# Performance work log

Measured on AMD Instinct MI355X. Metric: run time of the kernel, lower is better.

## Reference

```python
import jax, jax.numpy as jnp
import numpy as np

H = 1024          # h_dim
FF = 4 * H
E = 8             # num_expert
TOP_K = 2


def setup_inputs() -> dict:
    key = jax.random.key(0)
    ks = jax.random.split(key, 7)
    B, S = 4, 2048
    s = 0.02
    return {
        "x": jax.random.normal(ks[0], (B, S, H), dtype=jnp.float32),
        "Wg": jax.random.normal(ks[1], (H, E), dtype=jnp.float32) * s,
        "bg": jnp.zeros((E,), dtype=jnp.float32),
        "W1": jax.random.normal(ks[2], (E, H, FF), dtype=jnp.float32) * s,
        "b1": jnp.zeros((E, FF), dtype=jnp.float32),
        "W2": jax.random.normal(ks[3], (E, FF, H), dtype=jnp.float32) * s,
        "b2": jnp.zeros((E, H), dtype=jnp.float32),
    }


def _moe(x, Wg, bg, W1, b1, W2, b2):
    B, S, h = x.shape
    hs = x.reshape(-1, h)                                  # [T, H]
    logits = hs @ Wg + bg                                  # [T, E]
    probs = jax.nn.softmax(logits.astype(jnp.float32), axis=-1)
    w, idx = jax.lax.top_k(probs, TOP_K)                   # [T, K]
    w = jax.nn.softmax(w, axis=-1).astype(x.dtype)         # renormalize over top-k
    out = jnp.zeros_like(hs)
    for e in range(E):
        # per-token combine weight for expert e (0 if not selected)
        w_e = jnp.sum(w * (idx == e), axis=-1)             # [T]
        y = jax.nn.relu(hs @ W1[e] + b1[e]) @ W2[e] + b2[e]  # [T, H]
        out = out + w_e[:, None] * y
    return out.reshape(B, S, h), logits


def reference(x, Wg, bg, W1, b1, W2, b2):
    return _moe(x, Wg, bg, W1, b1, W2, b2)
```

## Files before the change

kernel.cpp:

```cpp
#include <hip/hip_runtime.h>
#include <hip/hip_bf16.h>

#define T_TOKENS 8192
#define HD 1024
#define FF 4096
#define NEXP 8
#define NR_MAX 17408

typedef __attribute__((ext_vector_type(8))) short bf16x8;
typedef __attribute__((ext_vector_type(4))) float f32x4;
typedef unsigned short ushort8v __attribute__((ext_vector_type(8)));

static __device__ __forceinline__ float b2f(ushort u) {
    union { unsigned u; float f; } c; c.u = ((unsigned)u) << 16; return c.f;
}
static __device__ __forceinline__ ushort f2b(float f) {
    union { float f; unsigned u; } c; c.f = f;
    unsigned r = c.u + 0x7fffu + ((c.u >> 16) & 1u);
    return (ushort)(r >> 16);
}

__global__ __launch_bounds__(256) void gate_kernel(
    const float* __restrict__ x, const float* __restrict__ Wg, const float* __restrict__ bg,
    float* __restrict__ logits, int* __restrict__ counts,
    int* __restrict__ e0a, int* __restrict__ e1a,
    float* __restrict__ w0a, float* __restrict__ w1a)
{
    int t = blockIdx.x * 4 + (threadIdx.x >> 6);
    int l = threadIdx.x & 63;
    const float* xr = x + (size_t)t * HD;
    float acc[8] = {0,0,0,0,0,0,0,0};
    #pragma unroll
    for (int i = 0; i < 4; ++i) {
        int h0 = i * 256 + l * 4;
        float4 xv = *(const float4*)(xr + h0);
        #pragma unroll
        for (int j = 0; j < 4; ++j) {
            float xs = (&xv.x)[j];
            const float4* wr = (const float4*)(Wg + (size_t)(h0 + j) * NEXP);
            float4 wa = wr[0], wb = wr[1];
            acc[0] = fmaf(xs, wa.x, acc[0]);
            acc[1] = fmaf(xs, wa.y, acc[1]);
            acc[2] = fmaf(xs, wa.z, acc[2]);
            acc[3] = fmaf(xs, wa.w, acc[3]);
            acc[4] = fmaf(xs, wb.x, acc[4]);
            acc[5] = fmaf(xs, wb.y, acc[5]);
            acc[6] = fmaf(xs, wb.z, acc[6]);
            acc[7] = fmaf(xs, wb.w, acc[7]);
        }
    }
    #pragma unroll
    for (int off = 32; off > 0; off >>= 1) {
        #pragma unroll
        for (int e = 0; e < 8; ++e) acc[e] += __shfl_down(acc[e], off, 64);
    }
    if (l == 0) {
        float lg[8];
        #pragma unroll
        for (int e = 0; e < 8; ++e) {
            lg[e] = acc[e] + bg[e];
            logits[(size_t)t * NEXP + e] = lg[e];
        }
        float m = lg[0];
        #pragma unroll
        for (int e = 1; e < 8; ++e) m = fmaxf(m, lg[e]);
        float p[8], s = 0.f;
        #pragma unroll
        for (int e = 0; e < 8; ++e) { p[e] = expf(lg[e] - m); s += p[e]; }
        float inv = 1.f / s;
        #pragma unroll
        for (int e = 0; e < 8; ++e) p[e] *= inv;
        int i0 = 0;
        #pragma unroll
        for (int e = 1; e < 8; ++e) if (p[e] > p[i0]) i0 = e;
        int i1 = (i0 == 0) ? 1 : 0;
        #pragma unroll
        for (int e = 0; e < 8; ++e) if (e != i0 && p[e] > p[i1]) i1 = e;
        float ed = expf(p[i1] - p[i0]);
        float w0 = 1.f / (1.f + ed);
        float w1 = ed / (1.f + ed);
        e0a[t] = i0; e1a[t] = i1; w0a[t] = w0; w1a[t] = w1;
        atomicAdd(&counts[i0], 1);
        atomicAdd(&counts[i1], 1);
    }
}

__global__ void offsets_kernel(const int* __restrict__ counts, int* __restrict__ off) {
    if (threadIdx.x == 0) {
        int o = 0;
        for (int e = 0; e < 8; ++e) { off[e] = o; o += (counts[e] + 127) & ~127; }
        off[8] = o;
    }
}

__global__ __launch_bounds__(256) void assign_kernel(
    const int* __restrict__ e0a, const int* __restrict__ e1a,
    const int* __restrict__ off, int* __restrict__ fill,
    int* __restrict__ row0, int* __restrict__ row1, int* __restrict__ row_token)
{
    int t = blockIdx.x * 256 + threadIdx.x;
    if (t >= T_TOKENS) return;
    int e0 = e0a[t];
    int r0 = off[e0] + atomicAdd(&fill[e0], 1);
    row0[t] = r0; row_token[r0] = t;
    int e1 = e1a[t];
    int r1 = off[e1] + atomicAdd(&fill[e1], 1);
    row1[t] = r1; row_token[r1] = t;
}

__global__ __launch_bounds__(256) void gather_kernel(
    const float* __restrict__ x, const int* __restrict__ row_token, ushort* __restrict__ Xp)
{
    int r = blockIdx.x;
    int tok = row_token[r];
    int c = threadIdx.x * 4;
    ushort4 o;
    if (tok >= 0 && tok < T_TOKENS) {
        float4 v = *(const float4*)(x + (size_t)tok * HD + c);
        o.x = f2b(v.x); o.y = f2b(v.y); o.z = f2b(v.z); o.w = f2b(v.w);
    } else {
        o.x = 0; o.y = 0; o.z = 0; o.w = 0;
    }
    *(ushort4*)(Xp + (size_t)r * HD + c) = o;
}

__global__ __launch_bounds__(256) void transpose_cvt_kernel(
    const float* __restrict__ in, ushort* __restrict__ out, int R, int C)
{
    __shared__ ushort tile[64][65];
    size_t esz = (size_t)R * C;
    const float* ein = in + (size_t)blockIdx.z * esz;
    ushort* eout = out + (size_t)blockIdx.z * esz;
    int c0 = blockIdx.x * 64, r0 = blockIdx.y * 64;
    int tr = threadIdx.x >> 4;
    int tc = (threadIdx.x & 15) * 4;
    #pragma unroll
    for (int i = 0; i < 4; ++i) {
        int r = tr + i * 16;
        float4 v = *(const float4*)(ein + (size_t)(r0 + r) * C + c0 + tc);
        tile[r][tc + 0] = f2b(v.x);
        tile[r][tc + 1] = f2b(v.y);
        tile[r][tc + 2] = f2b(v.z);
        tile[r][tc + 3] = f2b(v.w);
    }
    __syncthreads();
    int twc = threadIdx.x >> 3;
    int twr = (threadIdx.x & 7) * 8;
    #pragma unroll
    for (int i = 0; i < 2; ++i) {
        int cc = twc + i * 32;
        ushort8v v;
        #pragma unroll
        for (int j = 0; j < 8; ++j) v[j] = tile[twr + j][cc];
        *(ushort8v*)(eout + (size_t)(c0 + cc) * R + r0 + twr) = v;
    }
}

template<int K, int NTOT, bool RELU>
__global__ __launch_bounds__(256) void gemm_kernel(
    const ushort* __restrict__ A, const ushort* __restrict__ Bt,
    const float* __restrict__ bias, ushort* __restrict__ Out,
    const int* __restrict__ off)
{
    constexpr int NT = NTOT / 128;
    __shared__ __align__(16) ushort lds[2][2][128 * 32];

    int nwg = gridDim.x;
    int bid = blockIdx.x;
    int wgid = (bid & 7) * (nwg >> 3) + (bid >> 3);
    int ntile = wgid % NT;
    int mtile = wgid / NT;
    int r0 = mtile * 128;
    int total = off[8];
    if (r0 >= total) return;
    int e = 0;
    #pragma unroll
    for (int q = 0; q < 7; ++q) if (r0 >= off[q + 1]) e = q + 1;

    int tid = threadIdx.x;
    int w = tid >> 6, lane = tid & 63;
    int wr = w >> 1, wc = w & 1;
    int lr = lane & 15, lk = lane >> 4;

    const ushort* Ab = A + (size_t)r0 * K;
    const ushort* Bb = Bt + ((size_t)e * NTOT + (size_t)ntile * 128) * K;

    auto stage = [&](const ushort* gbase, ushort* ldsbase) {
        #pragma unroll
        for (int issue = 0; issue < 2; ++issue) {
            int row = issue * 64 + w * 16 + (lane >> 2);
            int chunk = (lane & 3) ^ ((lane >> 3) & 3);
            const ushort* g = gbase + (size_t)row * K + chunk * 8;
            ushort* lp = ldsbase + (issue * 64 + w * 16) * 32;
            __builtin_amdgcn_global_load_lds(
                (const __attribute__((address_space(1))) void*)g,
                (__attribute__((address_space(3))) void*)lp, 16, 0, 0);
        }
    };

    stage(Ab, &lds[0][0][0]);
    stage(Bb, &lds[0][1][0]);

    f32x4 acc[4][4];
    #pragma unroll
    for (int mi = 0; mi < 4; ++mi)
        #pragma unroll
        for (int ni = 0; ni < 4; ++ni) acc[mi][ni] = (f32x4){0.f, 0.f, 0.f, 0.f};

    __syncthreads();

    constexpr int KT = K / 32;
    int cur = 0;
    int slot = lk ^ ((lr >> 1) & 3);
    for (int kt = 0; kt < KT; ++kt) {
        if (kt + 1 < KT) {
            stage(Ab + (kt + 1) * 32, &lds[cur ^ 1][0][0]);
            stage(Bb + (kt + 1) * 32, &lds[cur ^ 1][1][0]);
        }
        const ushort* As = &lds[cur][0][0];
        const ushort* Bs = &lds[cur][1][0];
        bf16x8 a[4], b[4];
        #pragma unroll
        for (int mi = 0; mi < 4; ++mi)
            a[mi] = *(const bf16x8*)(As + (wr * 64 + mi * 16 + lr) * 32 + slot * 8);
        #pragma unroll
        for (int ni = 0; ni < 4; ++ni)
            b[ni] = *(const bf16x8*)(Bs + (wc * 64 + ni * 16 + lr) * 32 + slot * 8);
        #pragma unroll
        for (int mi = 0; mi < 4; ++mi)
            #pragma unroll
            for (int ni = 0; ni < 4; ++ni)
                acc[mi][ni] = __builtin_amdgcn_mfma_f32_16x16x32_bf16(
                    a[mi], b[ni], acc[mi][ni], 0, 0, 0);
        __syncthreads();
        cur ^= 1;
    }

    int c0 = ntile * 128 + wc * 64;
    int rbase = r0 + wr * 64;
    #pragma unroll
    for (int ni = 0; ni < 4; ++ni) {
        int n = c0 + ni * 16 + lr;
        float bv = bias[(size_t)e * NTOT + n];
        #pragma unroll
        for (int mi = 0; mi < 4; ++mi) {
            int m = rbase + mi * 16 + lk * 4;
            #pragma unroll
            for (int j = 0; j < 4; ++j) {
                float v = acc[mi][ni][j] + bv;
                if (RELU) v = fmaxf(v, 0.f);
                Out[(size_t)(m + j) * NTOT + n] = f2b(v);
            }
        }
    }
}

__global__ __launch_bounds__(256) void combine_kernel(
    const ushort* __restrict__ Y, const int* __restrict__ row0, const int* __restrict__ row1,
    const float* __restrict__ w0a, const float* __restrict__ w1a, float* __restrict__ out)
{
    int t = blockIdx.x;
    int c = threadIdx.x * 4;
    int r0 = row0[t], r1 = row1[t];
    float w0 = w0a[t], w1 = w1a[t];
    ushort4 ya = *(const ushort4*)(Y + (size_t)r0 * HD + c);
    ushort4 yb = *(const ushort4*)(Y + (size_t)r1 * HD + c);
    float4 o;
    o.x = w0 * b2f(ya.x) + w1 * b2f(yb.x);
    o.y = w0 * b2f(ya.y) + w1 * b2f(yb.y);
    o.z = w0 * b2f(ya.z) + w1 * b2f(yb.z);
    o.w = w0 * b2f(ya.w) + w1 * b2f(yb.w);
    *(float4*)(out + (size_t)t * HD + c) = o;
}

#define WSA(x) (((x) + 255) & ~(size_t)255)
static constexpr size_t OFF_COUNTS = 0;
static constexpr size_t OFF_FILL   = 64;
static constexpr size_t OFF_OFF    = 128;
static constexpr size_t OFF_E0     = 256;
static constexpr size_t OFF_E1     = OFF_E0 + (size_t)T_TOKENS * 4;
static constexpr size_t OFF_W0     = OFF_E1 + (size_t)T_TOKENS * 4;
static constexpr size_t OFF_W1A    = OFF_W0 + (size_t)T_TOKENS * 4;
static constexpr size_t OFF_R0     = OFF_W1A + (size_t)T_TOKENS * 4;
static constexpr size_t OFF_R1     = OFF_R0 + (size_t)T_TOKENS * 4;
static constexpr size_t OFF_RT     = OFF_R1 + (size_t)T_TOKENS * 4;
static constexpr size_t OFF_XP     = WSA(OFF_RT + (size_t)NR_MAX * 4);
static constexpr size_t OFF_W1T    = OFF_XP  + (size_t)NR_MAX * HD * 2;
static constexpr size_t OFF_W2T    = OFF_W1T + (size_t)NEXP * FF * HD * 2;
static constexpr size_t OFF_H1     = OFF_W2T + (size_t)NEXP * HD * FF * 2;
static constexpr size_t OFF_Y      = OFF_H1  + (size_t)NR_MAX * FF * 2;
static constexpr size_t WS_NEEDED  = OFF_Y   + (size_t)NR_MAX * HD * 2;

extern "C" void kernel_launch(void* const* d_in, const int* in_sizes, int n_in,
                              void* d_out, int out_size, void* d_ws, size_t ws_size,
                              hipStream_t stream) {
    (void)in_sizes; (void)n_in; (void)out_size;
    const float* x  = (const float*)d_in[0];
    const float* Wg = (const float*)d_in[1];
    const float* bg = (const float*)d_in[2];
    const float* W1 = (const float*)d_in[3];
    const float* b1 = (const float*)d_in[4];
    const float* W2 = (const float*)d_in[5];
    const float* b2 = (const float*)d_in[6];
    float* out    = (float*)d_out;
    float* logits = out + (size_t)T_TOKENS * HD;

    if (ws_size < WS_NEEDED) return;

    char* ws = (char*)d_ws;
    int*    counts = (int*)(ws + OFF_COUNTS);
    int*    fill   = (int*)(ws + OFF_FILL);
    int*    offp   = (int*)(ws + OFF_OFF);
    int*    e0a    = (int*)(ws + OFF_E0);
    int*    e1a    = (int*)(ws + OFF_E1);
    float*  w0a    = (float*)(ws + OFF_W0);
    float*  w1a    = (float*)(ws + OFF_W1A);
    int*    row0   = (int*)(ws + OFF_R0);
    int*    row1   = (int*)(ws + OFF_R1);
    int*    rowtok = (int*)(ws + OFF_RT);
    ushort* Xp     = (ushort*)(ws + OFF_XP);
    ushort* W1T    = (ushort*)(ws + OFF_W1T);
    ushort* W2T    = (ushort*)(ws + OFF_W2T);
    ushort* H1     = (ushort*)(ws + OFF_H1);
    ushort* Y      = (ushort*)(ws + OFF_Y);

    hipMemsetAsync(ws, 0, 256, stream);
    hipMemsetAsync(rowtok, 0xFF, (size_t)NR_MAX * 4, stream);

    gate_kernel<<<T_TOKENS / 4, 256, 0, stream>>>(x, Wg, bg, logits, counts, e0a, e1a, w0a, w1a);
    offsets_kernel<<<1, 64, 0, stream>>>(counts, offp);
    assign_kernel<<<T_TOKENS / 256, 256, 0, stream>>>(e0a, e1a, offp, fill, row0, row1, rowtok);
    gather_kernel<<<NR_MAX, 256, 0, stream>>>(x, rowtok, Xp);
    transpose_cvt_kernel<<<dim3(FF / 64, HD / 64, NEXP), 256, 0, stream>>>(W1, W1T, HD, FF);
    transpose_cvt_kernel<<<dim3(HD / 64, FF / 64, NEXP), 256, 0, stream>>>(W2, W2T, FF, HD);
    gemm_kernel<HD, FF, true>
        <<<(FF / 128) * (NR_MAX / 128), 256, 0, stream>>>(Xp, W1T, b1, H1, offp);
    gemm_kernel<FF, HD, false>
        <<<(HD / 128) * (NR_MAX / 128), 256, 0, stream>>>(H1, W2T, b2, Y, offp);
    combine_kernel<<<T_TOKENS, 256, 0, stream>>>(Y, row0, row1, w0a, w1a, out);
}
```

Baseline: 780.5 us.

## Widen GEMM tile to 128x256 with 512 threads and nontemporal H1 stores

The grouped expert GEMMs now use 128x256 output tiles computed by 8 waves (512 threads) instead of 128x128 with 4 waves. The B-operand staging is reworked into separate A and B LDS buffers with per-thread async global-to-LDS loads. Each loaded A tile is reused across twice as many output columns, which cuts redundant activation reads. The first GEMM also writes H1 with nontemporal stores. The trade is more LDS per block and fewer blocks per CU, and H1 may fall out of cache before the second GEMM reads it.

```diff
diff --git a/kernel.cpp b/kernel.cpp
--- a/kernel.cpp
+++ b/kernel.cpp
@@ -156,14 +156,16 @@
     }
 }
 
-template<int K, int NTOT, bool RELU>
-__global__ __launch_bounds__(256) void gemm_kernel(
+template<int K, int NTOT, bool RELU, bool NTSTORE>
+__global__ __launch_bounds__(512) void gemm_kernel(
     const ushort* __restrict__ A, const ushort* __restrict__ Bt,
     const float* __restrict__ bias, ushort* __restrict__ Out,
     const int* __restrict__ off)
 {
-    constexpr int NT = NTOT / 128;
-    __shared__ __align__(16) ushort lds[2][2][128 * 32];
+    constexpr int BN = 256;
+    constexpr int NT = NTOT / BN;
+    __shared__ __align__(16) ushort ldsA[2][128 * 32];
+    __shared__ __align__(16) ushort ldsB[2][BN * 32];
 
     int nwg = gridDim.x;
     int bid = blockIdx.x;
@@ -178,28 +180,33 @@
     for (int q = 0; q < 7; ++q) if (r0 >= off[q + 1]) e = q + 1;
 
     int tid = threadIdx.x;
-    int w = tid >> 6, lane = tid & 63;
-    int wr = w >> 1, wc = w & 1;
+    int wid = tid >> 6, lane = tid & 63;
+    int wr = wid >> 2, wc = wid & 3;
     int lr = lane & 15, lk = lane >> 4;
 
     const ushort* Ab = A + (size_t)r0 * K;
-    const ushort* Bb = Bt + ((size_t)e * NTOT + (size_t)ntile * 128) * K;
-
-    auto stage = [&](const ushort* gbase, ushort* ldsbase) {
-        #pragma unroll
-        for (int issue = 0; issue < 2; ++issue) {
-            int row = issue * 64 + w * 16 + (lane >> 2);
-            int chunk = (lane & 3) ^ ((lane >> 3) & 3);
-            const ushort* g = gbase + (size_t)row * K + chunk * 8;
-            ushort* lp = ldsbase + (issue * 64 + w * 16) * 32;
+    const ushort* Bb = Bt + ((size_t)e * NTOT + (size_t)ntile * BN) * K;
+
+    int srow = tid >> 2;
+    int schunk = (tid & 3) ^ ((tid >> 3) & 3);
+
+    auto stageA = [&](int kt, int buf) {
+        const ushort* g = Ab + (size_t)kt * 32 + (size_t)srow * K + schunk * 8;
+        __builtin_amdgcn_global_load_lds(
+            (const __attribute__((address_space(1))) void*)g,
+            (__attribute__((address_space(3))) void*)&ldsA[buf][tid * 8], 16, 0, 0);
+    };
+    auto stageB = [&](int kt, int buf) {
+        #pragma unroll
+        for (int i = 0; i < 2; ++i) {
+            const ushort* g = Bb + (size_t)kt * 32 + (size_t)(i * 128 + srow) * K + schunk * 8;
             __builtin_amdgcn_global_load_lds(
                 (const __attribute__((address_space(1))) void*)g,
-                (__attribute__((address_space(3))) void*)lp, 16, 0, 0);
+                (__attribute__((address_space(3))) void*)&ldsB[buf][i * 4096 + tid * 8], 16, 0, 0);
         }
     };
 
-    stage(Ab, &lds[0][0][0]);
-    stage(Bb, &lds[0][1][0]);
+    stageA(0, 0); stageB(0, 0);
 
     f32x4 acc[4][4];
     #pragma unroll
@@ -213,12 +220,9 @@
     int cur = 0;
     int slot = lk ^ ((lr >> 1) & 3);
     for (int kt = 0; kt < KT; ++kt) {
-        if (kt + 1 < KT) {
-            stage(Ab + (kt + 1) * 32, &lds[cur ^ 1][0][0]);
-            stage(Bb + (kt + 1) * 32, &lds[cur ^ 1][1][0]);
-        }
-        const ushort* As = &lds[cur][0][0];
-        const ushort* Bs = &lds[cur][1][0];
+        if (kt + 1 < KT) { stageA(kt + 1, cur ^ 1); stageB(kt + 1, cur ^ 1); }
+        const ushort* As = &ldsA[cur][0];
+        const ushort* Bs = &ldsB[cur][0];
         bf16x8 a[4], b[4];
         #pragma unroll
         for (int mi = 0; mi < 4; ++mi)
@@ -236,7 +240,7 @@
         cur ^= 1;
     }
 
-    int c0 = ntile * 128 + wc * 64;
+    int c0 = ntile * BN + wc * 64;
     int rbase = r0 + wr * 64;
     #pragma unroll
     for (int ni = 0; ni < 4; ++ni) {
@@ -249,7 +253,9 @@
             for (int j = 0; j < 4; ++j) {
                 float v = acc[mi][ni][j] + bv;
                 if (RELU) v = fmaxf(v, 0.f);
-                Out[(size_t)(m + j) * NTOT + n] = f2b(v);
+                ushort* p = &Out[(size_t)(m + j) * NTOT + n];
+                if (NTSTORE) __builtin_nontemporal_store(f2b(v), p);
+                else *p = f2b(v);
             }
         }
     }
@@ -333,9 +339,9 @@
     gather_kernel<<<NR_MAX, 256, 0, stream>>>(x, rowtok, Xp);
     transpose_cvt_kernel<<<dim3(FF / 64, HD / 64, NEXP), 256, 0, stream>>>(W1, W1T, HD, FF);
     transpose_cvt_kernel<<<dim3(HD / 64, FF / 64, NEXP), 256, 0, stream>>>(W2, W2T, FF, HD);
-    gemm_kernel<HD, FF, true>
-        <<<(FF / 128) * (NR_MAX / 128), 256, 0, stream>>>(Xp, W1T, b1, H1, offp);
-    gemm_kernel<FF, HD, false>
-        <<<(HD / 128) * (NR_MAX / 128), 256, 0, stream>>>(H1, W2T, b2, Y, offp);
+    gemm_kernel<HD, FF, true, true>
+        <<<(FF / 256) * (NR_MAX / 128), 512, 0, stream>>>(Xp, W1T, b1, H1, offp);
+    gemm_kernel<FF, HD, false, false>
+        <<<(HD / 256) * (NR_MAX / 128), 512, 0, stream>>>(H1, W2T, b2, Y, offp);
     combine_kernel<<<T_TOKENS, 256, 0, stream>>>(Y, row0, row1, w0a, w1a, out);
 }
```

New measurement: 893.3 us. 14.5% more time.

## Triple-buffer GEMM LDS tiles with two-deep prefetch and partial vmcnt waits

Applied to the files above, without the earlier changes.

The expert GEMM kernel moves from double-buffered to triple-buffered LDS staging. Global-to-LDS loads are now issued two K-steps ahead. Each step waits only until the next tile has landed (vmcnt(4)) instead of draining all loads with __syncthreads, so more memory latency can hide behind the MFMA work. The cost is LDS use per block rising from 32KB to 48KB, which may lower occupancy. The code also now relies on hand-written waitcnt and barrier ordering being correct.

```diff
diff --git a/kernel.cpp b/kernel.cpp
--- a/kernel.cpp
+++ b/kernel.cpp
@@ -163,7 +163,8 @@
     const int* __restrict__ off)
 {
     constexpr int NT = NTOT / 128;
-    __shared__ __align__(16) ushort lds[2][2][128 * 32];
+    constexpr int KT = K / 32;
+    __shared__ __align__(16) ushort lds[3][2][128 * 32];
 
     int nwg = gridDim.x;
     int bid = blockIdx.x;
@@ -185,38 +186,40 @@
     const ushort* Ab = A + (size_t)r0 * K;
     const ushort* Bb = Bt + ((size_t)e * NTOT + (size_t)ntile * 128) * K;
 
-    auto stage = [&](const ushort* gbase, ushort* ldsbase) {
+    auto stage = [&](int kt, int sl) {
         #pragma unroll
         for (int issue = 0; issue < 2; ++issue) {
             int row = issue * 64 + w * 16 + (lane >> 2);
             int chunk = (lane & 3) ^ ((lane >> 3) & 3);
-            const ushort* g = gbase + (size_t)row * K + chunk * 8;
-            ushort* lp = ldsbase + (issue * 64 + w * 16) * 32;
+            const ushort* ga = Ab + (size_t)kt * 32 + (size_t)row * K + chunk * 8;
+            const ushort* gb = Bb + (size_t)kt * 32 + (size_t)row * K + chunk * 8;
+            ushort* la = &lds[sl][0][(issue * 64 + w * 16) * 32];
+            ushort* lb = &lds[sl][1][(issue * 64 + w * 16) * 32];
             __builtin_amdgcn_global_load_lds(
-                (const __attribute__((address_space(1))) void*)g,
-                (__attribute__((address_space(3))) void*)lp, 16, 0, 0);
+                (const __attribute__((address_space(1))) void*)ga,
+                (__attribute__((address_space(3))) void*)la, 16, 0, 0);
+            __builtin_amdgcn_global_load_lds(
+                (const __attribute__((address_space(1))) void*)gb,
+                (__attribute__((address_space(3))) void*)lb, 16, 0, 0);
         }
     };
 
-    stage(Ab, &lds[0][0][0]);
-    stage(Bb, &lds[0][1][0]);
-
     f32x4 acc[4][4];
     #pragma unroll
     for (int mi = 0; mi < 4; ++mi)
         #pragma unroll
         for (int ni = 0; ni < 4; ++ni) acc[mi][ni] = (f32x4){0.f, 0.f, 0.f, 0.f};
 
-    __syncthreads();
-
-    constexpr int KT = K / 32;
-    int cur = 0;
+    stage(0, 0);
+    stage(1, 1);
+    asm volatile("s_waitcnt vmcnt(4)" ::: "memory");
+    __builtin_amdgcn_sched_barrier(0);
+    __builtin_amdgcn_s_barrier();
+
+    int cur = 0, nx2 = 2;
     int slot = lk ^ ((lr >> 1) & 3);
     for (int kt = 0; kt < KT; ++kt) {
-        if (kt + 1 < KT) {
-            stage(Ab + (kt + 1) * 32, &lds[cur ^ 1][0][0]);
-            stage(Bb + (kt + 1) * 32, &lds[cur ^ 1][1][0]);
-        }
+        if (kt + 2 < KT) stage(kt + 2, nx2);
         const ushort* As = &lds[cur][0][0];
         const ushort* Bs = &lds[cur][1][0];
         bf16x8 a[4], b[4];
@@ -232,8 +235,14 @@
             for (int ni = 0; ni < 4; ++ni)
                 acc[mi][ni] = __builtin_amdgcn_mfma_f32_16x16x32_bf16(
                     a[mi], b[ni], acc[mi][ni], 0, 0, 0);
-        __syncthreads();
-        cur ^= 1;
+        if (kt + 1 < KT) {
+            if (kt + 2 < KT) { asm volatile("s_waitcnt vmcnt(4)" ::: "memory"); }
+            else             { asm volatile("s_waitcnt vmcnt(0)" ::: "memory"); }
+            __builtin_amdgcn_sched_barrier(0);
+            __builtin_amdgcn_s_barrier();
+        }
+        cur = (cur == 2) ? 0 : cur + 1;
+        nx2 = (nx2 == 2) ? 0 : nx2 + 1;
     }
 
     int c0 = ntile * 128 + wc * 64;
```

Result: no change. 794.8 us (+1.8%).
